# Kernel tuning notes

Hardware: AMD Instinct MI355X
Metric: run time of the kernel (lower is better)

Reference implementation:

```python
import jax, jax.numpy as jnp
import numpy as np

INPUT_DIM, HIDDEN_DIM, OUTPUT_DIM = 64, 256, 32
BATCH, SEQ = 256, 1024
# AutoNCP(256, 32, sparsity_level=0.5): motor=32, command=max(int(0.4*224),1)=89, inter=135
LAYER_HID = [135, 89, 32]
LAYER_IN = [INPUT_DIM, 135, 89]


def setup_inputs() -> dict:
    key = jax.random.key(0)
    ks = iter(jax.random.split(key, 64))
    d = {}
    d["x"] = jax.random.normal(next(ks), (BATCH, SEQ, INPUT_DIM), dtype=jnp.float32)
    for l, (fin, hid) in enumerate(zip(LAYER_IN, LAYER_HID)):
        sp = jax.random.bernoulli(next(ks), 0.5, (hid, fin))
        d[f"mask{l}"] = jnp.concatenate([sp, jnp.ones((hid, hid), dtype=bool)], axis=1)
        scale = 1.0 / np.sqrt(fin + hid)
        for name in ("W1", "W2", "Wa", "Wb"):
            d[f"{name}_{l}"] = jax.random.normal(next(ks), (hid, fin + hid), dtype=jnp.float32) * scale
        for name in ("b1", "b2", "ba", "bb"):
            d[f"{name}_{l}"] = jnp.zeros((hid,), dtype=jnp.float32)
    d["fc_W"] = jax.random.normal(next(ks), (HIDDEN_DIM, HIDDEN_DIM), dtype=jnp.float32) * (1.0 / np.sqrt(HIDDEN_DIM))
    d["fc_b"] = jnp.zeros((HIDDEN_DIM,), dtype=jnp.float32)
    return d


def _cfc_cell(inp, h, mask, W1, b1, W2, b2, Wa, ba, Wb, bb):
    # ncps CfCCell, mode='default', no backbone, ts = 1.0
    x = jnp.concatenate([inp, h], axis=1)
    m = mask.astype(W1.dtype)
    ff1 = jnp.tanh(x @ (W1 * m).T + b1)
    ff2 = jnp.tanh(x @ (W2 * m).T + b2)
    t = jax.nn.sigmoid(x @ Wa.T + ba + x @ Wb.T + bb)  # sigmoid(t_a*ts + t_b), ts=1
    return ff1 * (1.0 - t) + t * ff2


def _forward(x, masks, layer_params, fc_W, fc_b):
    B = x.shape[0]
    init = tuple(jnp.zeros((B, h), dtype=x.dtype) for h in LAYER_HID)

    def step(carry, xt):
        hs = list(carry)
        inp = xt
        for l in range(3):  # inter -> command -> motor (WiredCfCCell)
            hs[l] = _cfc_cell(inp, hs[l], masks[l], *layer_params[l])
            inp = hs[l]
        return tuple(hs), None

    carry, _ = jax.lax.scan(step, init, jnp.swapaxes(x, 0, 1))  # scan over time [T,B,D]
    hn = jnp.concatenate(carry, axis=1)  # [B, HIDDEN_DIM] full state
    return hn @ fc_W.T + fc_b


def reference(x, mask0, mask1, mask2,
              W1_0, b1_0, W2_0, b2_0, Wa_0, ba_0, Wb_0, bb_0,
              W1_1, b1_1, W2_1, b2_1, Wa_1, ba_1, Wb_1, bb_1,
              W1_2, b1_2, W2_2, b2_2, Wa_2, ba_2, Wb_2, bb_2,
              fc_W, fc_b):
    masks = (mask0, mask1, mask2)
    lp = ((W1_0, b1_0, W2_0, b2_0, Wa_0, ba_0, Wb_0, bb_0),
          (W1_1, b1_1, W2_1, b2_1, Wa_1, ba_1, Wb_1, bb_1),
          (W1_2, b1_2, W2_2, b2_2, Wa_2, ba_2, Wb_2, bb_2))
    return _forward(x, masks, lp, fc_W, fc_b)
```

## Files before the change

kernel.cpp:

```cpp
#include <hip/hip_runtime.h>


typedef _Float16 half2v __attribute__((ext_vector_type(2)));
typedef _Float16 half8v __attribute__((ext_vector_type(8)));

#define NBLK   256
#define NTHR   1024
#define TSTEPS 1024
#define KPAD   224
#define KQ     56
#define NKB    7

struct Ptrs {
    const float* x;
    const unsigned int* msk[3];
    const float* W1[3];
    const float* W2[3];
    const float* Wa[3];
    const float* Wb[3];
    const float* b1[3];
    const float* b2[3];
    const float* ba[3];
    const float* bb[3];
    const float* fcW;
    const float* fcb;
};

__device__ __forceinline__ float fexp2(float x) {
#if __has_builtin(__builtin_amdgcn_exp2f)
    return __builtin_amdgcn_exp2f(x);
#else
    return exp2f(x);
#endif
}
__device__ __forceinline__ float frcp(float x) {
#if __has_builtin(__builtin_amdgcn_rcpf)
    return __builtin_amdgcn_rcpf(x);
#else
    return 1.0f / x;
#endif
}
__device__ __forceinline__ float fsig(float x) {
    return frcp(1.0f + fexp2(-1.442695041f * x));
}
__device__ __forceinline__ float ftanh(float x) {
    return 2.0f * frcp(1.0f + fexp2(-2.885390082f * x)) - 1.0f;
}

#if __has_builtin(__builtin_amdgcn_fdot2)
#define FD(a, b, c) __builtin_amdgcn_fdot2((a), (b), (c), false)
#else
__device__ __forceinline__ float fd_fallback(half2v a, half2v b, float c) {
    return c + (float)a[0] * (float)b[0] + (float)a[1] * (float)b[1];
}
#define FD(a, b, c) fd_fallback((a), (b), (c))
#endif

__global__ __launch_bounds__(NTHR)
__attribute__((amdgpu_waves_per_eu(4, 4)))
void cfc_kernel(Ptrs P, float* __restrict__ out) {
    __shared__ __align__(16) _Float16 xc[2][3][KPAD];
    __shared__ __align__(16) float hn[256];

    const int tid  = threadIdx.x;
    const int b    = blockIdx.x;
    const int unit = tid >> 2;
    const int q    = tid & 3;

    int L, n;
    if (unit < 135)      { L = 0; n = unit; }
    else if (unit < 224) { L = 1; n = unit - 135; }
    else                 { L = 2; n = unit - 224; }
    const int K    = (L == 0) ? 199 : ((L == 1) ? 224 : 121);
    const int HOFF = (L == 0) ? 0   : ((L == 1) ? 135 : 224);

    {
        int* z = (int*)&xc[0][0][0];
        for (int i = tid; i < 2 * 3 * KPAD / 2; i += NTHR) z[i] = 0;
    }
    __syncthreads();

    const int xlane = tid - 960;
    float xpend = 0.0f;
    if (xlane >= 0) {
        xc[0][0][xlane] = (_Float16)P.x[((size_t)b * TSTEPS + 0) * 64 + xlane];
        xpend           = P.x[((size_t)b * TSTEPS + 1) * 64 + xlane];
    }

    const float* W1p        = P.W1[L];
    const float* W2p        = P.W2[L];
    const float* Wap        = P.Wa[L];
    const float* Wbp        = P.Wb[L];
    const unsigned int* mkp = P.msk[L];
    const int nK   = n * K;
    const int koff = q * KQ;

    half2v wr1[KQ / 2], wr2[KQ / 2], wra[KQ / 2];
#pragma unroll
    for (int i = 0; i < KQ / 2; ++i) {
        const int k0 = koff + 2 * i, k1 = koff + 2 * i + 1;
        float u0 = 0.f, u1 = 0.f, v0 = 0.f, v1 = 0.f, a0 = 0.f, a1 = 0.f;
        if (k0 < K) {
            const int idx = nK + k0;
            const float mm = (mkp[idx] != 0u) ? 1.0f : 0.0f;
            u0 = W1p[idx] * mm;
            v0 = W2p[idx] * mm;
            a0 = Wap[idx] + Wbp[idx];
        }
        if (k1 < K) {
            const int idx = nK + k1;
            const float mm = (mkp[idx] != 0u) ? 1.0f : 0.0f;
            u1 = W1p[idx] * mm;
            v1 = W2p[idx] * mm;
            a1 = Wap[idx] + Wbp[idx];
        }
        wr1[i] = half2v{(_Float16)u0, (_Float16)u1};
        wr2[i] = half2v{(_Float16)v0, (_Float16)v1};
        wra[i] = half2v{(_Float16)a0, (_Float16)a1};
    }
    const float bv1 = P.b1[L][n];
    const float bv2 = P.b2[L][n];
    const float bva = P.ba[L][n] + P.bb[L][n];
    __syncthreads();

    for (int tick = 0; tick < TSTEPS + 2; ++tick) {
        if (xlane >= 0) {
            if (tick + 1 < TSTEPS)
                xc[(tick + 1) & 1][0][xlane] = (_Float16)xpend;
            if (tick + 2 < TSTEPS)
                xpend = P.x[((size_t)b * TSTEPS + (tick + 2)) * 64 + xlane];
        }

        const int s = tick - L;
        if (s >= 0 && s < TSTEPS) {
            const _Float16* src = &xc[s & 1][L][koff];
            float ac0 = 0.f, ac1 = 0.f, ac2 = 0.f, ac3 = 0.f, ac4 = 0.f, ac5 = 0.f;
#pragma unroll
            for (int kb = 0; kb < NKB; ++kb) {
                const half8v xv = *(const half8v*)(src + kb * 8);
                const half2v x0 = {xv[0], xv[1]};
                const half2v x1 = {xv[2], xv[3]};
                const half2v x2 = {xv[4], xv[5]};
                const half2v x3 = {xv[6], xv[7]};
                const int k4 = kb * 4;
                ac0 = FD(x0, wr1[k4 + 0], ac0);
                ac2 = FD(x0, wr2[k4 + 0], ac2);
                ac4 = FD(x0, wra[k4 + 0], ac4);
                ac1 = FD(x1, wr1[k4 + 1], ac1);
                ac3 = FD(x1, wr2[k4 + 1], ac3);
                ac5 = FD(x1, wra[k4 + 1], ac5);
                ac0 = FD(x2, wr1[k4 + 2], ac0);
                ac2 = FD(x2, wr2[k4 + 2], ac2);
                ac4 = FD(x2, wra[k4 + 2], ac4);
                ac1 = FD(x3, wr1[k4 + 3], ac1);
                ac3 = FD(x3, wr2[k4 + 3], ac3);
                ac5 = FD(x3, wra[k4 + 3], ac5);
            }
            float s1 = ac0 + ac1;
            float s2 = ac2 + ac3;
            float sa = ac4 + ac5;
            s1 += __shfl_xor(s1, 1, 64);
            s2 += __shfl_xor(s2, 1, 64);
            sa += __shfl_xor(sa, 1, 64);
            s1 += __shfl_xor(s1, 2, 64);
            s2 += __shfl_xor(s2, 2, 64);
            sa += __shfl_xor(sa, 2, 64);
            const float f1 = ftanh(s1 + bv1);
            const float f2 = ftanh(s2 + bv2);
            const float tg = fsig(sa + bva);
            const float h  = f1 + tg * (f2 - f1);
            const _Float16 hv = (_Float16)h;

            const int pA = s & 1;
            const int pB = (s + 1) & 1;
            if (q == 0) {
                if (L == 0)      xc[pA][1][n] = hv;
                else if (L == 1) xc[pA][2][n] = hv;
                if (s == TSTEPS - 1) hn[HOFF + n] = h;
            } else if (q == 1) {
                if (L == 0)      xc[pB][0][64 + n]  = hv;
                else if (L == 1) xc[pB][1][135 + n] = hv;
                else             xc[pB][2][89 + n]  = hv;
            }
        }
        __syncthreads();
    }

    {
        const int o = unit;
        const float4* wr = (const float4*)(P.fcW + (size_t)o * 256 + q * 64);
        const float4* hr = (const float4*)(hn + q * 64);
        float acc = (q == 0) ? P.fcb[o] : 0.0f;
#pragma unroll
        for (int d = 0; d < 16; ++d) {
            const float4 a = hr[d];
            const float4 w = wr[d];
            acc += a.x * w.x + a.y * w.y + a.z * w.z + a.w * w.w;
        }
        acc += __shfl_xor(acc, 1, 64);
        acc += __shfl_xor(acc, 2, 64);
        if (q == 0) out[(size_t)b * 256 + o] = acc;
    }
}

extern "C" void kernel_launch(void* const* d_in, const int* in_sizes, int n_in,
                              void* d_out, int out_size, void* d_ws, size_t ws_size,
                              hipStream_t stream) {
    (void)in_sizes; (void)n_in; (void)out_size; (void)d_ws; (void)ws_size;
    Ptrs P;
    P.x = (const float*)d_in[0];
    for (int l = 0; l < 3; ++l) {
        const int base = 1 + l * 9;
        P.msk[l] = (const unsigned int*)d_in[base + 0];
        P.W1[l]  = (const float*)d_in[base + 1];
        P.W2[l]  = (const float*)d_in[base + 2];
        P.Wa[l]  = (const float*)d_in[base + 3];
        P.Wb[l]  = (const float*)d_in[base + 4];
        P.b1[l]  = (const float*)d_in[base + 5];
        P.b2[l]  = (const float*)d_in[base + 6];
        P.ba[l]  = (const float*)d_in[base + 7];
        P.bb[l]  = (const float*)d_in[base + 8];
    }
    P.fcW = (const float*)d_in[28];
    P.fcb = (const float*)d_in[29];

    hipLaunchKernelGGL(cfc_kernel, dim3(NBLK), dim3(NTHR), 0, stream,
                       P, (float*)d_out);
}
```

Before: 1.712 ms.

## Halve threads per unit and spill part of weights to per-thread LDS

Each recurrent unit is now handled by 2 threads instead of 4 (512 threads per block), so each thread covers 112 K elements. W1 stays fully in registers, W2 is partly in registers and the rest plus the combined gate weights go to a per-thread slice of dynamic shared memory. This removes one shuffle-reduction stage and halves the thread count, but doubles the serial dot-product length per thread and adds LDS loads in the inner loop. The dynamic shared memory size (about 160KB) needs an attribute set at launch time.

```diff
diff --git a/kernel.cpp b/kernel.cpp
--- a/kernel.cpp
+++ b/kernel.cpp
@@ -4,12 +4,16 @@
 typedef _Float16 half2v __attribute__((ext_vector_type(2)));
 typedef _Float16 half8v __attribute__((ext_vector_type(8)));
 
-#define NBLK   256
-#define NTHR   1024
-#define TSTEPS 1024
-#define KPAD   224
-#define KQ     56
-#define NKB    7
+#define NBLK    256
+#define NTHR    512
+#define TSTEPS  1024
+#define KPAD    224
+#define KHALF   112
+#define NKB     14
+#define W2REG   10
+#define WSTRIDE 304
+#define WOFF    4096
+#define SMEM_BYTES (WOFF + NTHR * WSTRIDE)
 
 struct Ptrs {
     const float* x;
@@ -57,15 +61,16 @@
 #endif
 
 __global__ __launch_bounds__(NTHR)
-__attribute__((amdgpu_waves_per_eu(4, 4)))
+__attribute__((amdgpu_waves_per_eu(2)))
 void cfc_kernel(Ptrs P, float* __restrict__ out) {
-    __shared__ __align__(16) _Float16 xc[2][3][KPAD];
-    __shared__ __align__(16) float hn[256];
+    extern __shared__ __align__(16) char smem[];
+    _Float16 (*xc)[3][KPAD] = (_Float16 (*)[3][KPAD])smem;
+    float* hn = (float*)(smem + 2688);
 
     const int tid  = threadIdx.x;
     const int b    = blockIdx.x;
-    const int unit = tid >> 2;
-    const int q    = tid & 3;
+    const int unit = tid >> 1;
+    const int half = tid & 1;
 
     int L, n;
     if (unit < 135)      { L = 0; n = unit; }
@@ -75,12 +80,12 @@
     const int HOFF = (L == 0) ? 0   : ((L == 1) ? 135 : 224);
 
     {
-        int* z = (int*)&xc[0][0][0];
-        for (int i = tid; i < 2 * 3 * KPAD / 2; i += NTHR) z[i] = 0;
+        int* z = (int*)smem;
+        for (int i = tid; i < 2688 / 4; i += NTHR) z[i] = 0;
     }
     __syncthreads();
 
-    const int xlane = tid - 960;
+    const int xlane = tid - 448;
     float xpend = 0.0f;
     if (xlane >= 0) {
         xc[0][0][xlane] = (_Float16)P.x[((size_t)b * TSTEPS + 0) * 64 + xlane];
@@ -93,35 +98,55 @@
     const float* Wbp        = P.Wb[L];
     const unsigned int* mkp = P.msk[L];
     const int nK   = n * K;
-    const int koff = q * KQ;
-
-    half2v wr1[KQ / 2], wr2[KQ / 2], wra[KQ / 2];
-#pragma unroll
-    for (int i = 0; i < KQ / 2; ++i) {
+    const int koff = half * KHALF;
+
+    _Float16* wsl = (_Float16*)(smem + WOFF + tid * WSTRIDE);
+
+    half2v wr1[KHALF / 2], wr2[W2REG * 4];
+#pragma unroll
+    for (int i = 0; i < KHALF / 2; ++i) {
         const int k0 = koff + 2 * i, k1 = koff + 2 * i + 1;
-        float u0 = 0.f, u1 = 0.f, v0 = 0.f, v1 = 0.f, a0 = 0.f, a1 = 0.f;
-        if (k0 < K) {
-            const int idx = nK + k0;
-            const float mm = (mkp[idx] != 0u) ? 1.0f : 0.0f;
-            u0 = W1p[idx] * mm;
-            v0 = W2p[idx] * mm;
-            a0 = Wap[idx] + Wbp[idx];
-        }
-        if (k1 < K) {
-            const int idx = nK + k1;
-            const float mm = (mkp[idx] != 0u) ? 1.0f : 0.0f;
-            u1 = W1p[idx] * mm;
-            v1 = W2p[idx] * mm;
-            a1 = Wap[idx] + Wbp[idx];
-        }
+        float u0 = 0.f, u1 = 0.f;
+        if (k0 < K) { const int idx = nK + k0; u0 = mkp[idx] ? W1p[idx] : 0.f; }
+        if (k1 < K) { const int idx = nK + k1; u1 = mkp[idx] ? W1p[idx] : 0.f; }
         wr1[i] = half2v{(_Float16)u0, (_Float16)u1};
+    }
+#pragma unroll
+    for (int i = 0; i < W2REG * 4; ++i) {
+        const int k0 = koff + 2 * i, k1 = koff + 2 * i + 1;
+        float v0 = 0.f, v1 = 0.f;
+        if (k0 < K) { const int idx = nK + k0; v0 = mkp[idx] ? W2p[idx] : 0.f; }
+        if (k1 < K) { const int idx = nK + k1; v1 = mkp[idx] ? W2p[idx] : 0.f; }
         wr2[i] = half2v{(_Float16)v0, (_Float16)v1};
-        wra[i] = half2v{(_Float16)a0, (_Float16)a1};
+    }
+    for (int c = 0; c < NKB - W2REG; ++c) {
+        half8v w;
+#pragma unroll
+        for (int j = 0; j < 8; ++j) {
+            const int k = koff + (W2REG + c) * 8 + j;
+            float v = 0.f;
+            if (k < K) { const int idx = nK + k; v = mkp[idx] ? W2p[idx] : 0.f; }
+            w[j] = (_Float16)v;
+        }
+        *((half8v*)(wsl + c * 8)) = w;
+    }
+    for (int c = 0; c < NKB; ++c) {
+        half8v w;
+#pragma unroll
+        for (int j = 0; j < 8; ++j) {
+            const int k = koff + c * 8 + j;
+            float v = 0.f;
+            if (k < K) { const int idx = nK + k; v = Wap[idx] + Wbp[idx]; }
+            w[j] = (_Float16)v;
+        }
+        *((half8v*)(wsl + 32 + c * 8)) = w;
     }
     const float bv1 = P.b1[L][n];
     const float bv2 = P.b2[L][n];
     const float bva = P.ba[L][n] + P.bb[L][n];
     __syncthreads();
+
+    const _Float16* wa_l = wsl + 32;
 
     for (int tick = 0; tick < TSTEPS + 2; ++tick) {
         if (xlane >= 0) {
@@ -138,23 +163,40 @@
 #pragma unroll
             for (int kb = 0; kb < NKB; ++kb) {
                 const half8v xv = *(const half8v*)(src + kb * 8);
+                const half8v av = *(const half8v*)(wa_l + kb * 8);
                 const half2v x0 = {xv[0], xv[1]};
                 const half2v x1 = {xv[2], xv[3]};
                 const half2v x2 = {xv[4], xv[5]};
                 const half2v x3 = {xv[6], xv[7]};
+                const half2v a0 = {av[0], av[1]};
+                const half2v a1 = {av[2], av[3]};
+                const half2v a2 = {av[4], av[5]};
+                const half2v a3 = {av[6], av[7]};
                 const int k4 = kb * 4;
                 ac0 = FD(x0, wr1[k4 + 0], ac0);
-                ac2 = FD(x0, wr2[k4 + 0], ac2);
-                ac4 = FD(x0, wra[k4 + 0], ac4);
                 ac1 = FD(x1, wr1[k4 + 1], ac1);
-                ac3 = FD(x1, wr2[k4 + 1], ac3);
-                ac5 = FD(x1, wra[k4 + 1], ac5);
                 ac0 = FD(x2, wr1[k4 + 2], ac0);
-                ac2 = FD(x2, wr2[k4 + 2], ac2);
-                ac4 = FD(x2, wra[k4 + 2], ac4);
                 ac1 = FD(x3, wr1[k4 + 3], ac1);
-                ac3 = FD(x3, wr2[k4 + 3], ac3);
-                ac5 = FD(x3, wra[k4 + 3], ac5);
+                ac4 = FD(x0, a0, ac4);
+                ac5 = FD(x1, a1, ac5);
+                ac4 = FD(x2, a2, ac4);
+                ac5 = FD(x3, a3, ac5);
+                if (kb < W2REG) {
+                    ac2 = FD(x0, wr2[k4 + 0], ac2);
+                    ac3 = FD(x1, wr2[k4 + 1], ac3);
+                    ac2 = FD(x2, wr2[k4 + 2], ac2);
+                    ac3 = FD(x3, wr2[k4 + 3], ac3);
+                } else {
+                    const half8v wv = *(const half8v*)(wsl + (kb - W2REG) * 8);
+                    const half2v w0 = {wv[0], wv[1]};
+                    const half2v w1 = {wv[2], wv[3]};
+                    const half2v w2 = {wv[4], wv[5]};
+                    const half2v w3 = {wv[6], wv[7]};
+                    ac2 = FD(x0, w0, ac2);
+                    ac3 = FD(x1, w1, ac3);
+                    ac2 = FD(x2, w2, ac2);
+                    ac3 = FD(x3, w3, ac3);
+                }
             }
             float s1 = ac0 + ac1;
             float s2 = ac2 + ac3;
@@ -162,9 +204,6 @@
             s1 += __shfl_xor(s1, 1, 64);
             s2 += __shfl_xor(s2, 1, 64);
             sa += __shfl_xor(sa, 1, 64);
-            s1 += __shfl_xor(s1, 2, 64);
-            s2 += __shfl_xor(s2, 2, 64);
-            sa += __shfl_xor(sa, 2, 64);
             const float f1 = ftanh(s1 + bv1);
             const float f2 = ftanh(s2 + bv2);
             const float tg = fsig(sa + bva);
@@ -173,11 +212,11 @@
 
             const int pA = s & 1;
             const int pB = (s + 1) & 1;
-            if (q == 0) {
+            if (half == 0) {
                 if (L == 0)      xc[pA][1][n] = hv;
                 else if (L == 1) xc[pA][2][n] = hv;
                 if (s == TSTEPS - 1) hn[HOFF + n] = h;
-            } else if (q == 1) {
+            } else {
                 if (L == 0)      xc[pB][0][64 + n]  = hv;
                 else if (L == 1) xc[pB][1][135 + n] = hv;
                 else             xc[pB][2][89 + n]  = hv;
@@ -188,18 +227,17 @@
 
     {
         const int o = unit;
-        const float4* wr = (const float4*)(P.fcW + (size_t)o * 256 + q * 64);
-        const float4* hr = (const float4*)(hn + q * 64);
-        float acc = (q == 0) ? P.fcb[o] : 0.0f;
-#pragma unroll
-        for (int d = 0; d < 16; ++d) {
+        const float4* wr = (const float4*)(P.fcW + (size_t)o * 256 + half * 128);
+        const float4* hr = (const float4*)(hn + half * 128);
+        float acc = half ? 0.0f : P.fcb[o];
+#pragma unroll 8
+        for (int d = 0; d < 32; ++d) {
             const float4 a = hr[d];
             const float4 w = wr[d];
             acc += a.x * w.x + a.y * w.y + a.z * w.z + a.w * w.w;
         }
         acc += __shfl_xor(acc, 1, 64);
-        acc += __shfl_xor(acc, 2, 64);
-        if (q == 0) out[(size_t)b * 256 + o] = acc;
+        if (half == 0) out[(size_t)b * 256 + o] = acc;
     }
 }
 
@@ -224,6 +262,14 @@
     P.fcW = (const float*)d_in[28];
     P.fcb = (const float*)d_in[29];
 
-    hipLaunchKernelGGL(cfc_kernel, dim3(NBLK), dim3(NTHR), 0, stream,
+    static bool attr_set = false;
+    if (!attr_set) {
+        (void)hipFuncSetAttribute((const void*)cfc_kernel,
+                                  hipFuncAttributeMaxDynamicSharedMemorySize,
+                                  SMEM_BYTES);
+        attr_set = true;
+    }
+
+    hipLaunchKernelGGL(cfc_kernel, dim3(NBLK), dim3(NTHR), SMEM_BYTES, stream,
                        P, (float*)d_out);
 }
```

Result: faster. 1.643 ms (-4.0%).
